# Performance work log

Measured on AMD Instinct MI355X. Metric: run time of the kernel, lower is better.

## Reference

```python
import jax, jax.numpy as jnp
import numpy as np

ORDER = 24
N_POINTS = 524288


def setup_inputs() -> dict:
    key = jax.random.key(0)
    k1, k2 = jax.random.split(key)
    xyz = jax.random.uniform(k1, (N_POINTS, 3), dtype=jnp.float32)
    coeffs = jax.random.normal(k2, (ORDER ** 3,), dtype=jnp.float32) * 0.1
    return {"xyz": xyz, "coeffs": coeffs}


def reference(xyz, coeffs):
    # Faithful to: sum_{i,j,k} c[i,j,k] * sin(2pi i x) * sin(2pi j y) * sin(2pi k z)
    # but with per-axis sin tables computed once (O(order) transcendentals per point)
    # and the triple sum expressed as chained contractions (GEMM-like).
    order = ORDER
    C = coeffs.reshape(order, order, order)  # c[i,j,k]
    n = jnp.arange(order, dtype=xyz.dtype)   # frequencies 0..order-1 (i=0 row is all zeros)
    two_pi = jnp.asarray(2.0 * np.pi, dtype=xyz.dtype)
    S = jnp.sin(two_pi * xyz[:, :, None] * n)  # [N, 3, order]
    Sx, Sy, Sz = S[:, 0, :], S[:, 1, :], S[:, 2, :]  # each [N, order]
    A = jnp.einsum('nk,ijk->nij', Sz, C)   # [N, order, order]
    B = jnp.einsum('nj,nij->ni', Sy, A)    # [N, order]
    return jnp.einsum('ni,ni->n', Sx, B)   # [N]
```

## Files before the change

kernel.cpp:

```cpp
#include <hip/hip_runtime.h>

typedef _Float16 f16x2 __attribute__((ext_vector_type(2)));
typedef _Float16 f16x8 __attribute__((ext_vector_type(8)));
typedef float    f32x4 __attribute__((ext_vector_type(4)));

__global__ __launch_bounds__(256, 4) void fourier_mfma(
    const float* __restrict__ xyz,
    const float* __restrict__ coeffs,
    float* __restrict__ out)
{
    __shared__ __align__(16) unsigned short Bl[18944];

    const int tid  = threadIdx.x;
    const int wave = tid >> 6;
    const int lane = tid & 63;
    const int g    = lane >> 4;
    const int c    = lane & 15;

    for (int pass = 0; pass < 9; ++pass) {
        int chunk = pass * 256 + tid;
        int f  = chunk / 48, sl = chunk % 48;
        int s  = f >> 1,  tt = f & 1;
        int gg = sl >> 4, cc = sl & 15;
        int i  = 16 * tt + cc;
        f16x8 v;
        if (i < 24) {
            const float* src = coeffs + i * 576 + s * 24 + gg * 8;
#pragma unroll
            for (int e = 0; e < 8; ++e) v[e] = (_Float16)src[e];
        } else {
#pragma unroll
            for (int e = 0; e < 8; ++e) v[e] = (_Float16)0.f;
        }
        ((f16x8*)Bl)[chunk] = v;
    }

    const int gid = blockIdx.x * 4 + wave;
    const int p0  = gid * 64;

    float syp[4], syc[4], c2y[4];
    f16x2 sz2[4][4];
    const float kmask = (g < 3) ? 1.0f : 0.0f;

#pragma unroll
    for (int m = 0; m < 4; ++m) {
        int p = p0 + 16 * m + c;
        float y = xyz[3 * p + 1];
        float z = xyz[3 * p + 2];
        float sy1 = __builtin_amdgcn_sinf(y);
        float cy1 = __builtin_amdgcn_cosf(y);
        syp[m] = 0.0f; syc[m] = sy1; c2y[m] = 2.0f * cy1;
        float sz1 = __builtin_amdgcn_sinf(z);
        float cz1 = __builtin_amdgcn_cosf(z);
        float w   = __builtin_amdgcn_fractf((float)(8 * g) * z);
        float sb  = __builtin_amdgcn_sinf(w) * kmask;
        float cb  = __builtin_amdgcn_cosf(w);
        float c2z = 2.0f * cz1;
        float szf[8];
        szf[0] = sb;
        szf[1] = fmaf(sb, cz1, cb * sz1 * kmask);
#pragma unroll
        for (int e = 2; e < 8; ++e) szf[e] = fmaf(c2z, szf[e - 1], -szf[e - 2]);
#pragma unroll
        for (int q = 0; q < 4; ++q)
            sz2[m][q] = f16x2{(_Float16)szf[2 * q], (_Float16)szf[2 * q + 1]};
    }

    f32x4 acc[4][2] = {};

    __syncthreads();

    const int bslot = (lane < 48) ? lane : 47;
    const f16x8* Bf = (const f16x8*)Bl;

#pragma unroll
    for (int s = 1; s < 24; ++s) {
        f16x8 b0 = Bf[(2 * s + 0) * 48 + bslot];
        f16x8 b1 = Bf[(2 * s + 1) * 48 + bslot];
#pragma unroll
        for (int m = 0; m < 4; ++m) {
            _Float16 hy = (_Float16)syc[m];
            f16x2 hy2 = {hy, hy};
            f16x8 a;
#pragma unroll
            for (int q = 0; q < 4; ++q) {
                f16x2 pr = hy2 * sz2[m][q];
                a[2 * q]     = pr[0];
                a[2 * q + 1] = pr[1];
            }
            acc[m][0] = __builtin_amdgcn_mfma_f32_16x16x32_f16(a, b0, acc[m][0], 0, 0, 0);
            acc[m][1] = __builtin_amdgcn_mfma_f32_16x16x32_f16(a, b1, acc[m][1], 0, 0, 0);
            float nxt = fmaf(c2y[m], syc[m], -syp[m]);
            syp[m] = syc[m]; syc[m] = nxt;
        }
    }

    __syncthreads();

    float* T = (float*)Bl + wave * (64 * 37);
#pragma unroll
    for (int m = 0; m < 4; ++m)
#pragma unroll
        for (int t = 0; t < 2; ++t)
#pragma unroll
            for (int r = 0; r < 4; ++r) {
                int pr = 16 * m + 4 * g + r;
                int ii = 16 * t + c;
                T[pr * 37 + ii] = acc[m][t][r];
            }

    __syncthreads();

    {
        int p = p0 + lane;
        float x = xyz[3 * p];
        float sx1 = __builtin_amdgcn_sinf(x);
        float cx1 = __builtin_amdgcn_cosf(x);
        const float* Tr = T + lane * 37;
        float res = 0.0f;
        float sp = 0.0f, scur = sx1;
        const float c2x = 2.0f * cx1;
#pragma unroll
        for (int i = 1; i < 24; ++i) {
            res = fmaf(scur, Tr[i], res);
            float nx = fmaf(c2x, scur, -sp);
            sp = scur; scur = nx;
        }
        out[p] = res;
    }
}

extern "C" void kernel_launch(void* const* d_in, const int* in_sizes, int n_in,
                              void* d_out, int out_size, void* d_ws, size_t ws_size,
                              hipStream_t stream) {
    const float* xyz    = (const float*)d_in[0];
    const float* coeffs = (const float*)d_in[1];
    float* out = (float*)d_out;

    const int n = in_sizes[0] / 3;
    const int grid = n / 256;
    fourier_mfma<<<grid, 256, 0, stream>>>(xyz, coeffs, out);
}
```

Measured before the change: 35.73 us.

## Precompute fp16 coefficient tiles in a prep kernel and halve per-wave point tiles

```diff
diff --git a/kernel.cpp b/kernel.cpp
--- a/kernel.cpp
+++ b/kernel.cpp
@@ -2,14 +2,37 @@
 
 typedef _Float16 f16x2 __attribute__((ext_vector_type(2)));
 typedef _Float16 f16x8 __attribute__((ext_vector_type(8)));
+typedef __fp16   fp16v2 __attribute__((ext_vector_type(2)));
 typedef float    f32x4 __attribute__((ext_vector_type(4)));
 
-__global__ __launch_bounds__(256, 4) void fourier_mfma(
+#define TSTRIDE 21
+
+__global__ __launch_bounds__(256) void prep_B(const float* __restrict__ coeffs,
+                                              f16x8* __restrict__ wsB)
+{
+    int chunk = blockIdx.x * 256 + threadIdx.x;
+    int f  = chunk / 48, sl = chunk % 48;
+    int s  = f >> 1,  tt = f & 1;
+    int gg = sl >> 4, cc = sl & 15;
+    int i  = 16 * tt + cc;
+    f16x8 v;
+    if (i < 24) {
+        const float* src = coeffs + i * 576 + s * 24 + gg * 8;
+#pragma unroll
+        for (int e = 0; e < 8; ++e) v[e] = (_Float16)src[e];
+    } else {
+#pragma unroll
+        for (int e = 0; e < 8; ++e) v[e] = (_Float16)0.f;
+    }
+    wsB[chunk] = v;
+}
+
+__global__ __launch_bounds__(512, 8) void fourier_main(
     const float* __restrict__ xyz,
-    const float* __restrict__ coeffs,
+    const f16x8* __restrict__ wsB,
     float* __restrict__ out)
 {
-    __shared__ __align__(16) unsigned short Bl[18944];
+    __shared__ __align__(16) f16x8 Bl[2304];
 
     const int tid  = threadIdx.x;
     const int wave = tid >> 6;
@@ -17,45 +40,31 @@
     const int g    = lane >> 4;
     const int c    = lane & 15;
 
-    for (int pass = 0; pass < 9; ++pass) {
-        int chunk = pass * 256 + tid;
-        int f  = chunk / 48, sl = chunk % 48;
-        int s  = f >> 1,  tt = f & 1;
-        int gg = sl >> 4, cc = sl & 15;
-        int i  = 16 * tt + cc;
-        f16x8 v;
-        if (i < 24) {
-            const float* src = coeffs + i * 576 + s * 24 + gg * 8;
 #pragma unroll
-            for (int e = 0; e < 8; ++e) v[e] = (_Float16)src[e];
-        } else {
-#pragma unroll
-            for (int e = 0; e < 8; ++e) v[e] = (_Float16)0.f;
-        }
-        ((f16x8*)Bl)[chunk] = v;
-    }
+    for (int pass = 0; pass < 4; ++pass)
+        Bl[pass * 512 + tid] = wsB[pass * 512 + tid];
+    if (tid < 256) Bl[2048 + tid] = wsB[2048 + tid];
 
-    const int gid = blockIdx.x * 4 + wave;
-    const int p0  = gid * 64;
+    const int p0 = (blockIdx.x * 8 + wave) * 32;
 
-    float syp[4], syc[4], c2y[4];
-    f16x2 sz2[4][4];
+    float syp[2], syc[2], c2y[2];
+    f16x2 sz2[2][4];
     const float kmask = (g < 3) ? 1.0f : 0.0f;
 
 #pragma unroll
-    for (int m = 0; m < 4; ++m) {
+    for (int m = 0; m < 2; ++m) {
         int p = p0 + 16 * m + c;
         float y = xyz[3 * p + 1];
         float z = xyz[3 * p + 2];
         float sy1 = __builtin_amdgcn_sinf(y);
         float cy1 = __builtin_amdgcn_cosf(y);
-        syp[m] = 0.0f; syc[m] = sy1; c2y[m] = 2.0f * cy1;
+        syp[m] = 0.f; syc[m] = sy1; c2y[m] = 2.f * cy1;
         float sz1 = __builtin_amdgcn_sinf(z);
         float cz1 = __builtin_amdgcn_cosf(z);
-        float w   = __builtin_amdgcn_fractf((float)(8 * g) * z);
-        float sb  = __builtin_amdgcn_sinf(w) * kmask;
-        float cb  = __builtin_amdgcn_cosf(w);
-        float c2z = 2.0f * cz1;
+        float wv  = __builtin_amdgcn_fractf((float)(8 * g) * z);
+        float sb  = __builtin_amdgcn_sinf(wv) * kmask;
+        float cb  = __builtin_amdgcn_cosf(wv);
+        float c2z = 2.f * cz1;
         float szf[8];
         szf[0] = sb;
         szf[1] = fmaf(sb, cz1, cb * sz1 * kmask);
@@ -66,19 +75,17 @@
             sz2[m][q] = f16x2{(_Float16)szf[2 * q], (_Float16)szf[2 * q + 1]};
     }
 
-    f32x4 acc[4][2] = {};
+    f32x4 acc[2][2] = {};
 
     __syncthreads();
 
     const int bslot = (lane < 48) ? lane : 47;
-    const f16x8* Bf = (const f16x8*)Bl;
-
 #pragma unroll
     for (int s = 1; s < 24; ++s) {
-        f16x8 b0 = Bf[(2 * s + 0) * 48 + bslot];
-        f16x8 b1 = Bf[(2 * s + 1) * 48 + bslot];
+        f16x8 b0 = Bl[(2 * s + 0) * 48 + bslot];
+        f16x8 b1 = Bl[(2 * s + 1) * 48 + bslot];
 #pragma unroll
-        for (int m = 0; m < 4; ++m) {
+        for (int m = 0; m < 2; ++m) {
             _Float16 hy = (_Float16)syc[m];
             f16x2 hy2 = {hy, hy};
             f16x8 a;
@@ -97,36 +104,43 @@
 
     __syncthreads();
 
-    float* T = (float*)Bl + wave * (64 * 37);
+    unsigned int* Tw = (unsigned int*)Bl + wave * (32 * TSTRIDE);
 #pragma unroll
-    for (int m = 0; m < 4; ++m)
+    for (int m = 0; m < 2; ++m)
 #pragma unroll
-        for (int t = 0; t < 2; ++t)
-#pragma unroll
-            for (int r = 0; r < 4; ++r) {
-                int pr = 16 * m + 4 * g + r;
-                int ii = 16 * t + c;
-                T[pr * 37 + ii] = acc[m][t][r];
-            }
+        for (int r = 0; r < 4; ++r) {
+            int lr = 16 * m + 4 * g + r;
+            fp16v2 pk = __builtin_amdgcn_cvt_pkrtz(acc[m][0][r], acc[m][1][r]);
+            Tw[lr * TSTRIDE + c] = __builtin_bit_cast(unsigned int, pk);
+        }
 
     __syncthreads();
 
     {
-        int p = p0 + lane;
-        float x = xyz[3 * p];
-        float sx1 = __builtin_amdgcn_sinf(x);
-        float cx1 = __builtin_amdgcn_cosf(x);
-        const float* Tr = T + lane * 37;
-        float res = 0.0f;
-        float sp = 0.0f, scur = sx1;
-        const float c2x = 2.0f * cx1;
+        int lr = lane & 31;
+        int p  = p0 + lr;
+        float x   = xyz[3 * p];
+        float s1  = __builtin_amdgcn_sinf(x);
+        float c1  = __builtin_amdgcn_cosf(x);
+        float f16x_ = __builtin_amdgcn_fractf(16.f * x);
+        float s16 = __builtin_amdgcn_sinf(f16x_);
+        float c16 = __builtin_amdgcn_cosf(f16x_);
+        const float c2x = 2.f * c1;
+        float sA0 = 0.f,  sA1 = s1;
+        float sB0 = s16,  sB1 = fmaf(s16, c1, c16 * s1);
+        float res = 0.f;
+        const unsigned int* Tr = Tw + lr * TSTRIDE;
 #pragma unroll
-        for (int i = 1; i < 24; ++i) {
-            res = fmaf(scur, Tr[i], res);
-            float nx = fmaf(c2x, scur, -sp);
-            sp = scur; scur = nx;
+        for (int w = 0; w < 16; ++w) {
+            f16x2 h = __builtin_bit_cast(f16x2, Tr[w]);
+            res = fmaf(sA0, (float)h[0], res);
+            res = fmaf(sB0, (float)h[1], res);
+            float nA = fmaf(c2x, sA1, -sA0);
+            float nB = fmaf(c2x, sB1, -sB0);
+            sA0 = sA1; sA1 = nA;
+            sB0 = sB1; sB1 = nB;
         }
-        out[p] = res;
+        if (lane < 32) out[p] = res;
     }
 }
 
@@ -136,8 +150,11 @@
     const float* xyz    = (const float*)d_in[0];
     const float* coeffs = (const float*)d_in[1];
     float* out = (float*)d_out;
+    f16x8* wsB = (f16x8*)d_ws;
+
+    prep_B<<<9, 256, 0, stream>>>(coeffs, wsB);
 
     const int n = in_sizes[0] / 3;
     const int grid = n / 256;
-    fourier_mfma<<<grid, 256, 0, stream>>>(xyz, coeffs, out);
+    fourier_main<<<grid, 512, 0, stream>>>(xyz, wsB, out);
 }
```

After: 34.78 us. 2.7% less time.
